# Kernel tuning notes

Measured on AMD Instinct MI355X. Metric: run time of the kernel, lower is better.

Reference implementation:

```python
import jax, jax.numpy as jnp
import numpy as np

NB_OBJECTS = 3
DIM_BODY = 10
DIM_OBJECT = 15
DIM_ACT = 4
DIM_NODE = 128
D_PHI_IN = DIM_ACT + DIM_BODY + DIM_OBJECT + DIM_NODE  # 157
HID = 256
D_PHI_OUT = 3 * D_PHI_IN  # 471
D_RHO_OUT = 1
BATCH = 65536


def _linear_init(key, fan_in, fan_out):
    # torch nn.Linear default: U(-1/sqrt(fan_in), 1/sqrt(fan_in))
    bound = 1.0 / np.sqrt(fan_in)
    k1, k2 = jax.random.split(key)
    W = jax.random.uniform(k1, (fan_in, fan_out), minval=-bound, maxval=bound, dtype=jnp.float32)
    b = jax.random.uniform(k2, (fan_out,), minval=-bound, maxval=bound, dtype=jnp.float32)
    return W, b


def setup_inputs() -> dict:
    key = jax.random.key(0)
    ks = jax.random.split(key, 11)
    obs = jax.random.normal(ks[0], (BATCH, DIM_BODY + NB_OBJECTS * DIM_OBJECT), dtype=jnp.float32)
    act = jax.random.normal(ks[1], (BATCH, DIM_ACT), dtype=jnp.float32)
    nodes = jax.random.normal(ks[2], (NB_OBJECTS, BATCH, DIM_NODE), dtype=jnp.float32)
    phi1_w1, phi1_b1 = _linear_init(ks[3], D_PHI_IN, HID)
    phi1_w2, phi1_b2 = _linear_init(ks[4], HID, D_PHI_OUT)
    phi2_w1, phi2_b1 = _linear_init(ks[5], D_PHI_IN, HID)
    phi2_w2, phi2_b2 = _linear_init(ks[6], HID, D_PHI_OUT)
    rho1_w1, rho1_b1 = _linear_init(ks[7], D_PHI_OUT, HID)
    rho1_w2, rho1_b2 = _linear_init(ks[8], HID, D_RHO_OUT)
    rho2_w1, rho2_b1 = _linear_init(ks[9], D_PHI_OUT, HID)
    rho2_w2, rho2_b2 = _linear_init(ks[10], HID, D_RHO_OUT)
    return {
        "obs": obs, "act": act, "nodes": nodes,
        "phi1_w1": phi1_w1, "phi1_b1": phi1_b1, "phi1_w2": phi1_w2, "phi1_b2": phi1_b2,
        "phi2_w1": phi2_w1, "phi2_b1": phi2_b1, "phi2_w2": phi2_w2, "phi2_b2": phi2_b2,
        "rho1_w1": rho1_w1, "rho1_b1": rho1_b1, "rho1_w2": rho1_w2, "rho1_b2": rho1_b2,
        "rho2_w1": rho2_w1, "rho2_b1": rho2_b1, "rho2_w2": rho2_w2, "rho2_b2": rho2_b2,
    }


def reference(obs, act, nodes,
              phi1_w1, phi1_b1, phi1_w2, phi1_b2,
              phi2_w1, phi2_b1, phi2_w2, phi2_b2,
              rho1_w1, rho1_b1, rho1_w2, rho1_b2,
              rho2_w1, rho2_b1, rho2_w2, rho2_b2):
    B = obs.shape[0]
    obs_body = obs[:, :DIM_BODY]                                   # [B, 10]
    # per-object slices -> [nb_objects, B, dim_object]
    obs_obj = obs[:, DIM_BODY:].reshape(B, NB_OBJECTS, DIM_OBJECT).transpose(1, 0, 2)
    shared = jnp.concatenate([act, obs_body], axis=-1)             # [B, 14]
    shared = jnp.broadcast_to(shared[None], (NB_OBJECTS, B, shared.shape[-1]))
    inp_phi = jnp.concatenate([shared, obs_obj, nodes], axis=-1)   # [3, B, 157]

    def mlp2(x, w1, b1, w2, b2):
        h = jax.nn.relu(x @ w1 + b1)
        return jax.nn.relu(h @ w2 + b2)

    # DeepSet: per-entity phi then sum over entities
    out1 = mlp2(inp_phi, phi1_w1, phi1_b1, phi1_w2, phi1_b2).sum(axis=0)  # [B, 471]
    out2 = mlp2(inp_phi, phi2_w1, phi2_b1, phi2_w2, phi2_b2).sum(axis=0)
    q1 = jax.nn.relu(out1 @ rho1_w1 + rho1_b1) @ rho1_w2 + rho1_b2        # [B, 1]
    q2 = jax.nn.relu(out2 @ rho2_w1 + rho2_b1) @ rho2_w2 + rho2_b2
    return (q1, q2)
```

## Files before the change

kernel.cpp:

```cpp
#include <hip/hip_runtime.h>
#include <hip/hip_fp16.h>

typedef _Float16 half8 __attribute__((ext_vector_type(8)));
typedef float f32x4 __attribute__((ext_vector_type(4)));

#define BATCH 65536
#define M1 196608
#define K1 192

#define GLL16(g, l) __builtin_amdgcn_global_load_lds( \
    (const __attribute__((address_space(1))) unsigned int*)(const void*)(g), \
    (__attribute__((address_space(3))) unsigned int*)(void*)(l), 16, 0, 0)

__global__ void prep_kernel(const float* __restrict__ p1w1, const float* __restrict__ p2w1,
                            const float* __restrict__ p1w2, const float* __restrict__ p2w2,
                            const float* __restrict__ r1w1, const float* __restrict__ r2w1,
                            const float* __restrict__ p1b1, const float* __restrict__ p2b1,
                            const float* __restrict__ p1b2, const float* __restrict__ p2b2,
                            const float* __restrict__ rb1a, const float* __restrict__ rb1b,
                            _Float16* __restrict__ W1t, _Float16* __restrict__ W2t,
                            _Float16* __restrict__ R1t, float* __restrict__ b1cat,
                            float* __restrict__ b2cat, float* __restrict__ rbias) {
    int e = blockIdx.x * 256 + threadIdx.x;
    if (e < 98304) {
        int n = e / 192, c = e % 192;
        int k = (c < 128) ? (29 + c) : (c - 128);
        float v = 0.f;
        if (c < 128 || (c - 128) < 29) v = (n < 256) ? p1w1[k * 256 + n] : p2w1[k * 256 + (n - 256)];
        W1t[e] = (_Float16)v;
        return;
    }
    e -= 98304;
    if (e < 262144) {
        int net = e >> 17, rr = e & 131071;
        int n = rr >> 8, k = rr & 255;
        const float* w = net ? p2w2 : p1w2;
        W2t[(size_t)net * 131072 + rr] = (n < 471) ? (_Float16)w[k * 471 + n] : (_Float16)0.f;
        return;
    }
    e -= 262144;
    if (e < 262144) {
        int net = e >> 17, rr = e & 131071;
        int n = rr >> 9, k = rr & 511;
        const float* w = net ? r2w1 : r1w1;
        R1t[(size_t)net * 131072 + rr] = (k < 471) ? (_Float16)w[k * 256 + n] : (_Float16)0.f;
        return;
    }
    e -= 262144;
    if (e < 512) { b1cat[e] = (e < 256) ? p1b1[e] : p2b1[e - 256]; return; }
    e -= 512;
    if (e < 1024) {
        int net = e >> 9, n = e & 511;
        b2cat[e] = (n < 471) ? (net ? p2b2 : p1b2)[n] : 0.f;
        return;
    }
    e -= 1024;
    if (e < 512) {
        int net = e >> 8, n = e & 255;
        rbias[e] = (net ? rb1b : rb1a)[n];
    }
}

__global__ void build_x(const float* __restrict__ obs, const float* __restrict__ act,
                        const float* __restrict__ nodes, _Float16* __restrict__ Xh) {
    long idx = (long)blockIdx.x * 256 + threadIdx.x;
    int ch = (int)(idx % 24);
    long r = idx / 24;
    int o = (int)(r >> 16), b = (int)(r & 65535);
    half8 v;
    if (ch < 16) {
        const float* s = nodes + r * 128 + ch * 8;
#pragma unroll
        for (int j = 0; j < 8; ++j) v[j] = (_Float16)s[j];
    } else if (ch < 20) {
#pragma unroll
        for (int j = 0; j < 8; ++j) {
            int lc = ch * 8 + j - 128;
            float f = 0.f;
            if (lc < 4)       f = act[b * 4 + lc];
            else if (lc < 14) f = obs[b * 55 + (lc - 4)];
            else if (lc < 29) f = obs[b * 55 + 10 + o * 15 + (lc - 14)];
            v[j] = (_Float16)f;
        }
    } else {
#pragma unroll
        for (int j = 0; j < 8; ++j) v[j] = (_Float16)0.f;
    }
    *(half8*)(Xh + r * 192 + ch * 8) = v;
}


__global__ __launch_bounds__(256) void gemm1(const _Float16* __restrict__ Xh,
                                             const _Float16* __restrict__ W1t,
                                             const float* __restrict__ b1cat,
                                             _Float16* __restrict__ H) {
    __shared__ _Float16 As[2][4096];
    __shared__ _Float16 Bs[2][4096];
    const int tid = threadIdx.x;
    int bid = blockIdx.x;
    int w = (bid & 7) * 768 + (bid >> 3);
    const int m0 = (w >> 2) * 128, n0 = (w & 3) * 128;
    const _Float16* Ab = Xh + (long)m0 * K1;
    const _Float16* Bb = W1t + (long)n0 * K1;
    const int wid = tid >> 6, lane = tid & 63;
    const int lm = lane & 15, lq = lane >> 4;
    const int wr = (wid >> 1) * 64, wc = (wid & 1) * 64;
    const int srow = tid >> 2, schk = tid & 3;

    auto stage = [&](int s, int buf) {
        int ko = s * 32;
#pragma unroll
        for (int g = 0; g < 2; ++g) {
            int row = srow + g * 64, q = schk ^ ((row >> 1) & 3);
            GLL16(Ab + (long)row * K1 + ko + q * 8, &As[buf][0] + g * 2048 + wid * 512);
            GLL16(Bb + (long)row * K1 + ko + q * 8, &Bs[buf][0] + g * 2048 + wid * 512);
        }
    };

    stage(0, 0);
    __syncthreads();

    const int cc = (lq ^ ((lm >> 1) & 3)) * 8;
    f32x4 acc[4][4] = {};
    int cur = 0;
#pragma unroll
    for (int r = 0; r < 6; ++r) {
        if (r < 5) stage(r + 1, cur ^ 1);
        const _Float16* ab = &As[cur][0];
        const _Float16* bb = &Bs[cur][0];
        half8 a[4], b[4];
#pragma unroll
        for (int i = 0; i < 4; ++i) a[i] = *(const half8*)(ab + (wr + i * 16 + lm) * 32 + cc);
#pragma unroll
        for (int j = 0; j < 4; ++j) b[j] = *(const half8*)(bb + (wc + j * 16 + lm) * 32 + cc);
#pragma unroll
        for (int i = 0; i < 4; ++i)
#pragma unroll
            for (int j = 0; j < 4; ++j)
                acc[i][j] = __builtin_amdgcn_mfma_f32_16x16x32_f16(a[i], b[j], acc[i][j], 0, 0, 0);
        __syncthreads();
        cur ^= 1;
    }
#pragma unroll
    for (int j = 0; j < 4; ++j) {
        int n = n0 + wc + j * 16 + lm;
        int net = n >> 8, ncol = n & 255;
        float bi = b1cat[n];
        _Float16* hp = H + (long)net * ((long)M1 * 256) + ncol;
#pragma unroll
        for (int i = 0; i < 4; ++i) {
            int mrow = m0 + wr + i * 16 + lq * 4;
#pragma unroll
            for (int rg = 0; rg < 4; ++rg) {
                float v = acc[i][j][rg] + bi;
                v = v > 0.f ? v : 0.f;
                hp[(long)(mrow + rg) * 256] = (_Float16)v;
            }
        }
    }
}

__global__ __launch_bounds__(256) void gemm_sum(const _Float16* __restrict__ H,
                                                const _Float16* __restrict__ W2t,
                                                const float* __restrict__ b2cat,
                                                _Float16* __restrict__ Osum) {
    __shared__ _Float16 As[2][4096];
    __shared__ _Float16 Bs[2][4096];
    const int tid = threadIdx.x;
    int bid = blockIdx.x;
    int w = (bid & 7) * 512 + (bid >> 3);
    const int n0 = (w & 3) * 128, net = (w >> 2) & 1, b0 = (w >> 3) * 128;
    const _Float16* Ab = H + (long)net * ((long)M1 * 256) + (long)b0 * 256;
    const _Float16* Bb = W2t + (long)net * 131072 + (long)n0 * 256;
    const float* bp = b2cat + net * 512;
    const int wid = tid >> 6, lane = tid & 63;
    const int lm = lane & 15, lq = lane >> 4;
    const int wr = (wid >> 1) * 64, wc = (wid & 1) * 64;
    const int srow = tid >> 2, schk = tid & 3;

    float bi[4];
#pragma unroll
    for (int j = 0; j < 4; ++j) bi[j] = bp[n0 + wc + j * 16 + lm];

    auto stage = [&](int s, int buf) {
        int obj = s >> 3, ko = (s & 7) * 32;
#pragma unroll
        for (int g = 0; g < 2; ++g) {
            int row = srow + g * 64, q = schk ^ ((row >> 1) & 3);
            GLL16(Ab + ((long)obj * BATCH + row) * 256 + ko + q * 8, &As[buf][0] + g * 2048 + wid * 512);
            GLL16(Bb + (long)row * 256 + ko + q * 8, &Bs[buf][0] + g * 2048 + wid * 512);
        }
    };

    stage(0, 0);
    __syncthreads();

    const int cc = (lq ^ ((lm >> 1) & 3)) * 8;
    f32x4 acc[4][4] = {};
    f32x4 sum[4][4] = {};
    int cur = 0;
    for (int r = 0; r < 24; ++r) {
        if (r < 23) stage(r + 1, cur ^ 1);
        const _Float16* ab = &As[cur][0];
        const _Float16* bb = &Bs[cur][0];
        half8 a[4], b[4];
#pragma unroll
        for (int i = 0; i < 4; ++i) a[i] = *(const half8*)(ab + (wr + i * 16 + lm) * 32 + cc);
#pragma unroll
        for (int j = 0; j < 4; ++j) b[j] = *(const half8*)(bb + (wc + j * 16 + lm) * 32 + cc);
#pragma unroll
        for (int i = 0; i < 4; ++i)
#pragma unroll
            for (int j = 0; j < 4; ++j)
                acc[i][j] = __builtin_amdgcn_mfma_f32_16x16x32_f16(a[i], b[j], acc[i][j], 0, 0, 0);
        if ((r & 7) == 7) {
#pragma unroll
            for (int i = 0; i < 4; ++i)
#pragma unroll
                for (int j = 0; j < 4; ++j) {
#pragma unroll
                    for (int rg = 0; rg < 4; ++rg) {
                        float v = acc[i][j][rg] + bi[j];
                        sum[i][j][rg] += (v > 0.f ? v : 0.f);
                    }
                    acc[i][j] = f32x4{0.f, 0.f, 0.f, 0.f};
                }
        }
        __syncthreads();
        cur ^= 1;
    }
    _Float16* op = Osum + (long)net * ((long)BATCH * 512);
#pragma unroll
    for (int j = 0; j < 4; ++j) {
        int n = n0 + wc + j * 16 + lm;
#pragma unroll
        for (int i = 0; i < 4; ++i) {
            int mrow = b0 + wr + i * 16 + lq * 4;
#pragma unroll
            for (int rg = 0; rg < 4; ++rg)
                op[(long)(mrow + rg) * 512 + n] = (_Float16)sum[i][j][rg];
        }
    }
}

__global__ __launch_bounds__(512) void gemm3q(const _Float16* __restrict__ Osum,
                                              const _Float16* __restrict__ R1t,
                                              const float* __restrict__ rbias,
                                              const float* __restrict__ r1w2,
                                              const float* __restrict__ r2w2,
                                              const float* __restrict__ r1b2,
                                              const float* __restrict__ r2b2,
                                              float* __restrict__ out) {
    __shared__ _Float16 As[2][4096];
    __shared__ _Float16 Bs[2][8192];
    __shared__ float qlds[128];
    const int tid = threadIdx.x;
    int bid = blockIdx.x;
    int w = (bid & 7) * 128 + (bid >> 3);
    const int net = w & 1, b0 = (w >> 1) * 128;
    if (tid < 128) qlds[tid] = 0.f;
    const _Float16* Ab = Osum + (long)net * ((long)BATCH * 512) + (long)b0 * 512;
    const _Float16* Bb = R1t + (long)net * 131072;
    const int wid = tid >> 6, lane = tid & 63;
    const int lm = lane & 15, lq = lane >> 4;
    const int wr = (wid >> 2) * 64, wc = (wid & 3) * 64;
    const int srow = tid >> 2, schk = tid & 3;

    auto stage = [&](int s, int buf) {
        int ko = s * 32;
        {
            int row = srow, q = schk ^ ((row >> 1) & 3);
            GLL16(Ab + (long)row * 512 + ko + q * 8, &As[buf][0] + wid * 512);
        }
#pragma unroll
        for (int g = 0; g < 2; ++g) {
            int row = srow + g * 128, q = schk ^ ((row >> 1) & 3);
            GLL16(Bb + (long)row * 512 + ko + q * 8, &Bs[buf][0] + g * 4096 + wid * 512);
        }
    };

    stage(0, 0);
    __syncthreads();

    const int cc = (lq ^ ((lm >> 1) & 3)) * 8;
    f32x4 acc[4][4] = {};
    int cur = 0;
    for (int r = 0; r < 16; ++r) {
        if (r < 15) stage(r + 1, cur ^ 1);
        const _Float16* ab = &As[cur][0];
        const _Float16* bb = &Bs[cur][0];
        half8 a[4], b[4];
#pragma unroll
        for (int i = 0; i < 4; ++i) a[i] = *(const half8*)(ab + (wr + i * 16 + lm) * 32 + cc);
#pragma unroll
        for (int j = 0; j < 4; ++j) b[j] = *(const half8*)(bb + (wc + j * 16 + lm) * 32 + cc);
#pragma unroll
        for (int i = 0; i < 4; ++i)
#pragma unroll
            for (int j = 0; j < 4; ++j)
                acc[i][j] = __builtin_amdgcn_mfma_f32_16x16x32_f16(a[i], b[j], acc[i][j], 0, 0, 0);
        __syncthreads();
        cur ^= 1;
    }
    const float* w2 = net ? r2w2 : r1w2;
    const float* rb = rbias + net * 256;
    float w2v[4], bv[4];
#pragma unroll
    for (int j = 0; j < 4; ++j) {
        int col = wc + j * 16 + lm;
        w2v[j] = w2[col];
        bv[j] = rb[col];
    }
    f32x4 qp[4] = {};
#pragma unroll
    for (int i = 0; i < 4; ++i)
#pragma unroll
        for (int j = 0; j < 4; ++j)
#pragma unroll
            for (int rg = 0; rg < 4; ++rg) {
                float v = acc[i][j][rg] + bv[j];
                v = v > 0.f ? v : 0.f;
                qp[i][rg] += v * w2v[j];
            }
#pragma unroll
    for (int d = 1; d < 16; d <<= 1)
#pragma unroll
        for (int i = 0; i < 4; ++i)
#pragma unroll
            for (int rg = 0; rg < 4; ++rg)
                qp[i][rg] += __shfl_xor(qp[i][rg], d, 64);
    if ((lane & 15) == 0) {
#pragma unroll
        for (int i = 0; i < 4; ++i)
#pragma unroll
            for (int rg = 0; rg < 4; ++rg)
                atomicAdd(&qlds[wr + i * 16 + lq * 4 + rg], qp[i][rg]);
    }
    __syncthreads();
    if (tid < 128)
        out[(long)net * BATCH + b0 + tid] = qlds[tid] + (net ? r2b2[0] : r1b2[0]);
}

extern "C" void kernel_launch(void* const* d_in, const int* in_sizes, int n_in,
                              void* d_out, int out_size, void* d_ws, size_t ws_size,
                              hipStream_t stream) {
    const float* obs  = (const float*)d_in[0];
    const float* act  = (const float*)d_in[1];
    const float* nodes= (const float*)d_in[2];
    const float* p1w1 = (const float*)d_in[3];  const float* p1b1 = (const float*)d_in[4];
    const float* p1w2 = (const float*)d_in[5];  const float* p1b2 = (const float*)d_in[6];
    const float* p2w1 = (const float*)d_in[7];  const float* p2b1 = (const float*)d_in[8];
    const float* p2w2 = (const float*)d_in[9];  const float* p2b2 = (const float*)d_in[10];
    const float* r1w1 = (const float*)d_in[11]; const float* r1b1 = (const float*)d_in[12];
    const float* r1w2 = (const float*)d_in[13]; const float* r1b2 = (const float*)d_in[14];
    const float* r2w1 = (const float*)d_in[15]; const float* r2b1 = (const float*)d_in[16];
    const float* r2w2 = (const float*)d_in[17]; const float* r2b2 = (const float*)d_in[18];

    const size_t oW1t  = 0;
    const size_t oW2t  = 196608;
    const size_t oR1t  = 720896;
    const size_t oB1   = 1245184;
    const size_t oB2   = 1247232;
    const size_t oRB   = 1251328;
    const size_t oXO   = 1253376;
    const size_t oH    = 135471104;
    const size_t need  = 336797696;
    if (ws_size < need) return;

    char* ws = (char*)d_ws;
    _Float16* W1t  = (_Float16*)(ws + oW1t);
    _Float16* W2t  = (_Float16*)(ws + oW2t);
    _Float16* R1t  = (_Float16*)(ws + oR1t);
    float*    b1cat= (float*)(ws + oB1);
    float*    b2cat= (float*)(ws + oB2);
    float*    rbias= (float*)(ws + oRB);
    _Float16* Xh   = (_Float16*)(ws + oXO);
    _Float16* Osum = (_Float16*)(ws + oXO);
    _Float16* H    = (_Float16*)(ws + oH);
    float* out = (float*)d_out;

    prep_kernel<<<2440, 256, 0, stream>>>(p1w1, p2w1, p1w2, p2w2, r1w1, r2w1,
                                          p1b1, p2b1, p1b2, p2b2, r1b1, r2b1,
                                          W1t, W2t, R1t, b1cat, b2cat, rbias);
    build_x<<<18432, 256, 0, stream>>>(obs, act, nodes, Xh);
    gemm1<<<6144, 256, 0, stream>>>(Xh, W1t, b1cat, H);
    gemm_sum<<<4096, 256, 0, stream>>>(H, W2t, b2cat, Osum);
    gemm3q<<<1024, 512, 0, stream>>>(Osum, R1t, rbias, r1w2, r2w2, r1b2, r2b2, out);
}
```

Measured before the change: 391.5 us.

## Keep weight panel resident in LDS with persistent blocks and triple-buffered A streaming

```diff
diff --git a/kernel.cpp b/kernel.cpp
--- a/kernel.cpp
+++ b/kernel.cpp
@@ -11,6 +11,10 @@
 #define GLL16(g, l) __builtin_amdgcn_global_load_lds( \
     (const __attribute__((address_space(1))) unsigned int*)(const void*)(g), \
     (__attribute__((address_space(3))) unsigned int*)(void*)(l), 16, 0, 0)
+
+#define WAIT_VM1() asm volatile("s_waitcnt vmcnt(1)" ::: "memory")
+#define WAIT_VM0() asm volatile("s_waitcnt vmcnt(0)" ::: "memory")
+#define SBAR() do { __builtin_amdgcn_s_barrier(); __builtin_amdgcn_sched_barrier(0); } while (0)
 
 __global__ void prep_kernel(const float* __restrict__ p1w1, const float* __restrict__ p2w1,
                             const float* __restrict__ p1w2, const float* __restrict__ p2w2,
@@ -22,15 +26,15 @@
                             _Float16* __restrict__ R1t, float* __restrict__ b1cat,
                             float* __restrict__ b2cat, float* __restrict__ rbias) {
     int e = blockIdx.x * 256 + threadIdx.x;
-    if (e < 98304) {
-        int n = e / 192, c = e % 192;
+    if (e < 131072) {
+        int n = e >> 8, c = e & 255;
         int k = (c < 128) ? (29 + c) : (c - 128);
         float v = 0.f;
-        if (c < 128 || (c - 128) < 29) v = (n < 256) ? p1w1[k * 256 + n] : p2w1[k * 256 + (n - 256)];
+        if (c < 157) v = (n < 256) ? p1w1[k * 256 + n] : p2w1[k * 256 + (n - 256)];
         W1t[e] = (_Float16)v;
         return;
     }
-    e -= 98304;
+    e -= 131072;
     if (e < 262144) {
         int net = e >> 17, rr = e & 131071;
         int n = rr >> 8, k = rr & 255;
@@ -90,155 +94,171 @@
 }
 
 
-__global__ __launch_bounds__(256) void gemm1(const _Float16* __restrict__ Xh,
+__global__ __launch_bounds__(512) void gemm1(const _Float16* __restrict__ Xh,
                                              const _Float16* __restrict__ W1t,
                                              const float* __restrict__ b1cat,
                                              _Float16* __restrict__ H) {
-    __shared__ _Float16 As[2][4096];
-    __shared__ _Float16 Bs[2][4096];
+    __shared__ _Float16 Bp[65536];
+    __shared__ _Float16 Ar[3][4096];
     const int tid = threadIdx.x;
-    int bid = blockIdx.x;
-    int w = (bid & 7) * 768 + (bid >> 3);
-    const int m0 = (w >> 2) * 128, n0 = (w & 3) * 128;
-    const _Float16* Ab = Xh + (long)m0 * K1;
-    const _Float16* Bb = W1t + (long)n0 * K1;
+    const int bid = blockIdx.x;
+    const int nhalf = bid & 1;
+    const int mset = bid >> 1;
+    const int MT = 6, R = 6, TOT = 36;
     const int wid = tid >> 6, lane = tid & 63;
     const int lm = lane & 15, lq = lane >> 4;
-    const int wr = (wid >> 1) * 64, wc = (wid & 1) * 64;
-    const int srow = tid >> 2, schk = tid & 3;
-
-    auto stage = [&](int s, int buf) {
-        int ko = s * 32;
-#pragma unroll
-        for (int g = 0; g < 2; ++g) {
-            int row = srow + g * 64, q = schk ^ ((row >> 1) & 3);
-            GLL16(Ab + (long)row * K1 + ko + q * 8, &As[buf][0] + g * 2048 + wid * 512);
-            GLL16(Bb + (long)row * K1 + ko + q * 8, &Bs[buf][0] + g * 2048 + wid * 512);
-        }
+    const int wr = (wid >> 2) * 64, wc = (wid & 3) * 64;
+
+    {
+        const _Float16* src = W1t + (long)nhalf * 65536;
+#pragma unroll
+        for (int it = 0; it < 16; ++it) {
+            int row = it * 16 + (tid >> 5);
+            int q = (tid & 31) ^ (row & 7);
+            GLL16(src + (long)row * 256 + q * 8, &Bp[0] + it * 4096 + wid * 512);
+        }
+    }
+    const int arow = tid >> 2, asch = tid & 3;
+    const int aq = asch ^ ((arow >> 1) & 3);
+    auto stageA = [&](int g) {
+        int mt = g / R, s = g - mt * R;
+        int m0 = (mset * MT + mt) * 128;
+        GLL16(Xh + (long)(m0 + arow) * K1 + s * 32 + aq * 8, &Ar[g % 3][0] + wid * 512);
     };
-
-    stage(0, 0);
-    __syncthreads();
+    stageA(0); stageA(1);
 
     const int cc = (lq ^ ((lm >> 1) & 3)) * 8;
-    f32x4 acc[4][4] = {};
-    int cur = 0;
-#pragma unroll
-    for (int r = 0; r < 6; ++r) {
-        if (r < 5) stage(r + 1, cur ^ 1);
-        const _Float16* ab = &As[cur][0];
-        const _Float16* bb = &Bs[cur][0];
-        half8 a[4], b[4];
-#pragma unroll
-        for (int i = 0; i < 4; ++i) a[i] = *(const half8*)(ab + (wr + i * 16 + lm) * 32 + cc);
-#pragma unroll
-        for (int j = 0; j < 4; ++j) b[j] = *(const half8*)(bb + (wc + j * 16 + lm) * 32 + cc);
-#pragma unroll
-        for (int i = 0; i < 4; ++i)
-#pragma unroll
-            for (int j = 0; j < 4; ++j)
-                acc[i][j] = __builtin_amdgcn_mfma_f32_16x16x32_f16(a[i], b[j], acc[i][j], 0, 0, 0);
-        __syncthreads();
-        cur ^= 1;
-    }
-#pragma unroll
-    for (int j = 0; j < 4; ++j) {
-        int n = n0 + wc + j * 16 + lm;
-        int net = n >> 8, ncol = n & 255;
-        float bi = b1cat[n];
-        _Float16* hp = H + (long)net * ((long)M1 * 256) + ncol;
-#pragma unroll
-        for (int i = 0; i < 4; ++i) {
-            int mrow = m0 + wr + i * 16 + lq * 4;
-#pragma unroll
-            for (int rg = 0; rg < 4; ++rg) {
-                float v = acc[i][j][rg] + bi;
-                v = v > 0.f ? v : 0.f;
-                hp[(long)(mrow + rg) * 256] = (_Float16)v;
+    const int bxr = lm & 7;
+    float bi[4];
+#pragma unroll
+    for (int j = 0; j < 4; ++j) bi[j] = b1cat[nhalf * 256 + wc + j * 16 + lm];
+    _Float16* hp0 = H + (long)nhalf * ((long)M1 * 256);
+
+    int rr = 0;
+    for (int mt = 0; mt < MT; ++mt) {
+        f32x4 acc[4][4] = {};
+        for (int s = 0; s < R; ++s, ++rr) {
+            if (rr + 1 < TOT) { WAIT_VM1(); } else { WAIT_VM0(); }
+            SBAR();
+            if (rr + 2 < TOT) stageA(rr + 2);
+            const _Float16* ab = &Ar[rr % 3][0];
+            half8 a[4], b[4];
+#pragma unroll
+            for (int i = 0; i < 4; ++i) a[i] = *(const half8*)(ab + (wr + i * 16 + lm) * 32 + cc);
+            int bc = ((s * 4 + lq) ^ bxr) * 8;
+#pragma unroll
+            for (int j = 0; j < 4; ++j) b[j] = *(const half8*)(&Bp[0] + (wc + j * 16 + lm) * 256 + bc);
+#pragma unroll
+            for (int i = 0; i < 4; ++i)
+#pragma unroll
+                for (int j = 0; j < 4; ++j)
+                    acc[i][j] = __builtin_amdgcn_mfma_f32_16x16x32_f16(a[i], b[j], acc[i][j], 0, 0, 0);
+        }
+        int m0 = (mset * MT + mt) * 128;
+#pragma unroll
+        for (int j = 0; j < 4; ++j) {
+            int ncol = wc + j * 16 + lm;
+#pragma unroll
+            for (int i = 0; i < 4; ++i) {
+                int mrow = m0 + wr + i * 16 + lq * 4;
+#pragma unroll
+                for (int rg = 0; rg < 4; ++rg) {
+                    float v = acc[i][j][rg] + bi[j];
+                    v = v > 0.f ? v : 0.f;
+                    hp0[(long)(mrow + rg) * 256 + ncol] = (_Float16)v;
+                }
             }
         }
     }
 }
 
-__global__ __launch_bounds__(256) void gemm_sum(const _Float16* __restrict__ H,
+__global__ __launch_bounds__(512) void gemm_sum(const _Float16* __restrict__ H,
                                                 const _Float16* __restrict__ W2t,
                                                 const float* __restrict__ b2cat,
                                                 _Float16* __restrict__ Osum) {
-    __shared__ _Float16 As[2][4096];
-    __shared__ _Float16 Bs[2][4096];
+    __shared__ _Float16 Bp[65536];
+    __shared__ _Float16 Ar[3][4096];
     const int tid = threadIdx.x;
-    int bid = blockIdx.x;
-    int w = (bid & 7) * 512 + (bid >> 3);
-    const int n0 = (w & 3) * 128, net = (w >> 2) & 1, b0 = (w >> 3) * 128;
-    const _Float16* Ab = H + (long)net * ((long)M1 * 256) + (long)b0 * 256;
-    const _Float16* Bb = W2t + (long)net * 131072 + (long)n0 * 256;
-    const float* bp = b2cat + net * 512;
+    const int bid = blockIdx.x;
+    const int net = bid & 1, nhalf = (bid >> 1) & 1, mset = bid >> 2;
+    const int MT = 4, R = 24, TOT = 96;
+    const int n0 = nhalf * 256;
     const int wid = tid >> 6, lane = tid & 63;
     const int lm = lane & 15, lq = lane >> 4;
-    const int wr = (wid >> 1) * 64, wc = (wid & 1) * 64;
-    const int srow = tid >> 2, schk = tid & 3;
-
+    const int wr = (wid >> 2) * 64, wc = (wid & 3) * 64;
+    const _Float16* Hb = H + (long)net * ((long)M1 * 256);
+
+    {
+        const _Float16* src = W2t + (long)net * 131072 + (long)n0 * 256;
+#pragma unroll
+        for (int it = 0; it < 16; ++it) {
+            int row = it * 16 + (tid >> 5);
+            int q = (tid & 31) ^ (row & 7);
+            GLL16(src + (long)row * 256 + q * 8, &Bp[0] + it * 4096 + wid * 512);
+        }
+    }
+    const int arow = tid >> 2, asch = tid & 3;
+    const int aq = asch ^ ((arow >> 1) & 3);
+    auto stageA = [&](int g) {
+        int mt = g / R, s = g - mt * R;
+        int obj = s >> 3, ko = (s & 7) * 32;
+        int m0 = (mset * MT + mt) * 128;
+        GLL16(Hb + ((long)(obj * BATCH + m0 + arow)) * 256 + ko + aq * 8, &Ar[g % 3][0] + wid * 512);
+    };
+    stageA(0); stageA(1);
+
+    const int cc = (lq ^ ((lm >> 1) & 3)) * 8;
+    const int bxr = lm & 7;
     float bi[4];
 #pragma unroll
-    for (int j = 0; j < 4; ++j) bi[j] = bp[n0 + wc + j * 16 + lm];
-
-    auto stage = [&](int s, int buf) {
-        int obj = s >> 3, ko = (s & 7) * 32;
-#pragma unroll
-        for (int g = 0; g < 2; ++g) {
-            int row = srow + g * 64, q = schk ^ ((row >> 1) & 3);
-            GLL16(Ab + ((long)obj * BATCH + row) * 256 + ko + q * 8, &As[buf][0] + g * 2048 + wid * 512);
-            GLL16(Bb + (long)row * 256 + ko + q * 8, &Bs[buf][0] + g * 2048 + wid * 512);
-        }
-    };
-
-    stage(0, 0);
-    __syncthreads();
-
-    const int cc = (lq ^ ((lm >> 1) & 3)) * 8;
-    f32x4 acc[4][4] = {};
-    f32x4 sum[4][4] = {};
-    int cur = 0;
-    for (int r = 0; r < 24; ++r) {
-        if (r < 23) stage(r + 1, cur ^ 1);
-        const _Float16* ab = &As[cur][0];
-        const _Float16* bb = &Bs[cur][0];
-        half8 a[4], b[4];
-#pragma unroll
-        for (int i = 0; i < 4; ++i) a[i] = *(const half8*)(ab + (wr + i * 16 + lm) * 32 + cc);
-#pragma unroll
-        for (int j = 0; j < 4; ++j) b[j] = *(const half8*)(bb + (wc + j * 16 + lm) * 32 + cc);
-#pragma unroll
-        for (int i = 0; i < 4; ++i)
-#pragma unroll
-            for (int j = 0; j < 4; ++j)
-                acc[i][j] = __builtin_amdgcn_mfma_f32_16x16x32_f16(a[i], b[j], acc[i][j], 0, 0, 0);
-        if ((r & 7) == 7) {
+    for (int j = 0; j < 4; ++j) bi[j] = b2cat[net * 512 + n0 + wc + j * 16 + lm];
+    _Float16* op = Osum + (long)net * ((long)BATCH * 512);
+
+    int rr = 0;
+    for (int mt = 0; mt < MT; ++mt) {
+        f32x4 acc[4][4] = {};
+        f32x4 sum[4][4] = {};
+        for (int s = 0; s < R; ++s, ++rr) {
+            if (rr + 1 < TOT) { WAIT_VM1(); } else { WAIT_VM0(); }
+            SBAR();
+            if (rr + 2 < TOT) stageA(rr + 2);
+            const _Float16* ab = &Ar[rr % 3][0];
+            half8 a[4], b[4];
+#pragma unroll
+            for (int i = 0; i < 4; ++i) a[i] = *(const half8*)(ab + (wr + i * 16 + lm) * 32 + cc);
+            int bc = (((s & 7) * 4 + lq) ^ bxr) * 8;
+#pragma unroll
+            for (int j = 0; j < 4; ++j) b[j] = *(const half8*)(&Bp[0] + (wc + j * 16 + lm) * 256 + bc);
 #pragma unroll
             for (int i = 0; i < 4; ++i)
 #pragma unroll
-                for (int j = 0; j < 4; ++j) {
-#pragma unroll
-                    for (int rg = 0; rg < 4; ++rg) {
-                        float v = acc[i][j][rg] + bi[j];
-                        sum[i][j][rg] += (v > 0.f ? v : 0.f);
+                for (int j = 0; j < 4; ++j)
+                    acc[i][j] = __builtin_amdgcn_mfma_f32_16x16x32_f16(a[i], b[j], acc[i][j], 0, 0, 0);
+            if ((s & 7) == 7) {
+#pragma unroll
+                for (int i = 0; i < 4; ++i)
+#pragma unroll
+                    for (int j = 0; j < 4; ++j) {
+#pragma unroll
+                        for (int rg = 0; rg < 4; ++rg) {
+                            float v = acc[i][j][rg] + bi[j];
+                            sum[i][j][rg] += (v > 0.f ? v : 0.f);
+                        }
+                        acc[i][j] = f32x4{0.f, 0.f, 0.f, 0.f};
                     }
-                    acc[i][j] = f32x4{0.f, 0.f, 0.f, 0.f};
-                }
-        }
-        __syncthreads();
-        cur ^= 1;
-    }
-    _Float16* op = Osum + (long)net * ((long)BATCH * 512);
-#pragma unroll
-    for (int j = 0; j < 4; ++j) {
-        int n = n0 + wc + j * 16 + lm;
-#pragma unroll
-        for (int i = 0; i < 4; ++i) {
-            int mrow = b0 + wr + i * 16 + lq * 4;
-#pragma unroll
-            for (int rg = 0; rg < 4; ++rg)
-                op[(long)(mrow + rg) * 512 + n] = (_Float16)sum[i][j][rg];
+            }
+        }
+        int m0 = (mset * MT + mt) * 128;
+#pragma unroll
+        for (int j = 0; j < 4; ++j) {
+            int n = n0 + wc + j * 16 + lm;
+#pragma unroll
+            for (int i = 0; i < 4; ++i) {
+                int mrow = m0 + wr + i * 16 + lq * 4;
+#pragma unroll
+                for (int rg = 0; rg < 4; ++rg)
+                    op[(long)(mrow + rg) * 512 + n] = (_Float16)sum[i][j][rg];
+            }
         }
     }
 }
@@ -251,8 +271,8 @@
                                               const float* __restrict__ r1b2,
                                               const float* __restrict__ r2b2,
                                               float* __restrict__ out) {
-    __shared__ _Float16 As[2][4096];
-    __shared__ _Float16 Bs[2][8192];
+    __shared__ _Float16 As[2][8192];
+    __shared__ _Float16 Bs[2][16384];
     __shared__ float qlds[128];
     const int tid = threadIdx.x;
     int bid = blockIdx.x;
@@ -264,17 +284,19 @@
     const int wid = tid >> 6, lane = tid & 63;
     const int lm = lane & 15, lq = lane >> 4;
     const int wr = (wid >> 2) * 64, wc = (wid & 3) * 64;
-    const int srow = tid >> 2, schk = tid & 3;
+    const int xv = lm & 7;
+    const int srow = tid >> 3, schk = tid & 7;
 
     auto stage = [&](int s, int buf) {
-        int ko = s * 32;
-        {
-            int row = srow, q = schk ^ ((row >> 1) & 3);
-            GLL16(Ab + (long)row * 512 + ko + q * 8, &As[buf][0] + wid * 512);
-        }
+        int ko = s * 64;
 #pragma unroll
         for (int g = 0; g < 2; ++g) {
-            int row = srow + g * 128, q = schk ^ ((row >> 1) & 3);
+            int row = srow + g * 64, q = schk ^ (row & 7);
+            GLL16(Ab + (long)row * 512 + ko + q * 8, &As[buf][0] + g * 4096 + wid * 512);
+        }
+#pragma unroll
+        for (int g = 0; g < 4; ++g) {
+            int row = srow + g * 64, q = schk ^ (row & 7);
             GLL16(Bb + (long)row * 512 + ko + q * 8, &Bs[buf][0] + g * 4096 + wid * 512);
         }
     };
@@ -282,23 +304,26 @@
     stage(0, 0);
     __syncthreads();
 
-    const int cc = (lq ^ ((lm >> 1) & 3)) * 8;
     f32x4 acc[4][4] = {};
     int cur = 0;
-    for (int r = 0; r < 16; ++r) {
-        if (r < 15) stage(r + 1, cur ^ 1);
+    for (int r = 0; r < 8; ++r) {
+        if (r < 7) stage(r + 1, cur ^ 1);
         const _Float16* ab = &As[cur][0];
         const _Float16* bb = &Bs[cur][0];
-        half8 a[4], b[4];
-#pragma unroll
-        for (int i = 0; i < 4; ++i) a[i] = *(const half8*)(ab + (wr + i * 16 + lm) * 32 + cc);
-#pragma unroll
-        for (int j = 0; j < 4; ++j) b[j] = *(const half8*)(bb + (wc + j * 16 + lm) * 32 + cc);
-#pragma unroll
-        for (int i = 0; i < 4; ++i)
-#pragma unroll
-            for (int j = 0; j < 4; ++j)
-                acc[i][j] = __builtin_amdgcn_mfma_f32_16x16x32_f16(a[i], b[j], acc[i][j], 0, 0, 0);
+#pragma unroll
+        for (int ks = 0; ks < 2; ++ks) {
+            const int off = ((ks * 4 + lq) ^ xv) * 8;
+            half8 a[4], b[4];
+#pragma unroll
+            for (int i = 0; i < 4; ++i) a[i] = *(const half8*)(ab + (wr + i * 16 + lm) * 64 + off);
+#pragma unroll
+            for (int j = 0; j < 4; ++j) b[j] = *(const half8*)(bb + (wc + j * 16 + lm) * 64 + off);
+#pragma unroll
+            for (int i = 0; i < 4; ++i)
+#pragma unroll
+                for (int j = 0; j < 4; ++j)
+                    acc[i][j] = __builtin_amdgcn_mfma_f32_16x16x32_f16(a[i], b[j], acc[i][j], 0, 0, 0);
+        }
         __syncthreads();
         cur ^= 1;
     }
@@ -357,14 +382,14 @@
     const float* r2w2 = (const float*)d_in[17]; const float* r2b2 = (const float*)d_in[18];
 
     const size_t oW1t  = 0;
-    const size_t oW2t  = 196608;
-    const size_t oR1t  = 720896;
-    const size_t oB1   = 1245184;
-    const size_t oB2   = 1247232;
-    const size_t oRB   = 1251328;
-    const size_t oXO   = 1253376;
-    const size_t oH    = 135471104;
-    const size_t need  = 336797696;
+    const size_t oW2t  = 262144;
+    const size_t oR1t  = 786432;
+    const size_t oB1   = 1310720;
+    const size_t oB2   = 1312768;
+    const size_t oRB   = 1316864;
+    const size_t oXO   = 1318912;
+    const size_t oH    = 135536640;
+    const size_t need  = 336863232;
     if (ws_size < need) return;
 
     char* ws = (char*)d_ws;
@@ -379,11 +404,11 @@
     _Float16* H    = (_Float16*)(ws + oH);
     float* out = (float*)d_out;
 
-    prep_kernel<<<2440, 256, 0, stream>>>(p1w1, p2w1, p1w2, p2w2, r1w1, r2w1,
+    prep_kernel<<<2568, 256, 0, stream>>>(p1w1, p2w1, p1w2, p2w2, r1w1, r2w1,
                                           p1b1, p2b1, p1b2, p2b2, r1b1, r2b1,
                                           W1t, W2t, R1t, b1cat, b2cat, rbias);
     build_x<<<18432, 256, 0, stream>>>(obs, act, nodes, Xh);
-    gemm1<<<6144, 256, 0, stream>>>(Xh, W1t, b1cat, H);
-    gemm_sum<<<4096, 256, 0, stream>>>(H, W2t, b2cat, Osum);
+    gemm1<<<512, 512, 0, stream>>>(Xh, W1t, b1cat, H);
+    gemm_sum<<<512, 512, 0, stream>>>(H, W2t, b2cat, Osum);
     gemm3q<<<1024, 512, 0, stream>>>(Osum, R1t, rbias, r1w2, r2w2, r1b2, r2b2, out);
 }
```

Result: faster. 378.7 us (-3.3%).

## Trim layer-1 K padding and double K-tile depth in gemm_sum and gemm3q

Applied to the files above, without the earlier changes.

```diff
diff --git a/kernel.cpp b/kernel.cpp
--- a/kernel.cpp
+++ b/kernel.cpp
@@ -6,7 +6,7 @@
 
 #define BATCH 65536
 #define M1 196608
-#define K1 192
+#define K1 160
 
 #define GLL16(g, l) __builtin_amdgcn_global_load_lds( \
     (const __attribute__((address_space(1))) unsigned int*)(const void*)(g), \
@@ -22,15 +22,15 @@
                             _Float16* __restrict__ R1t, float* __restrict__ b1cat,
                             float* __restrict__ b2cat, float* __restrict__ rbias) {
     int e = blockIdx.x * 256 + threadIdx.x;
-    if (e < 98304) {
-        int n = e / 192, c = e % 192;
+    if (e < 81920) {
+        int n = e / 160, c = e % 160;
         int k = (c < 128) ? (29 + c) : (c - 128);
         float v = 0.f;
-        if (c < 128 || (c - 128) < 29) v = (n < 256) ? p1w1[k * 256 + n] : p2w1[k * 256 + (n - 256)];
+        if (c < 157) v = (n < 256) ? p1w1[k * 256 + n] : p2w1[k * 256 + (n - 256)];
         W1t[e] = (_Float16)v;
         return;
     }
-    e -= 98304;
+    e -= 81920;
     if (e < 262144) {
         int net = e >> 17, rr = e & 131071;
         int n = rr >> 8, k = rr & 255;
@@ -64,15 +64,15 @@
 __global__ void build_x(const float* __restrict__ obs, const float* __restrict__ act,
                         const float* __restrict__ nodes, _Float16* __restrict__ Xh) {
     long idx = (long)blockIdx.x * 256 + threadIdx.x;
-    int ch = (int)(idx % 24);
-    long r = idx / 24;
+    int ch = (int)(idx % 20);
+    long r = idx / 20;
     int o = (int)(r >> 16), b = (int)(r & 65535);
     half8 v;
     if (ch < 16) {
         const float* s = nodes + r * 128 + ch * 8;
 #pragma unroll
         for (int j = 0; j < 8; ++j) v[j] = (_Float16)s[j];
-    } else if (ch < 20) {
+    } else {
 #pragma unroll
         for (int j = 0; j < 8; ++j) {
             int lc = ch * 8 + j - 128;
@@ -82,11 +82,8 @@
             else if (lc < 29) f = obs[b * 55 + 10 + o * 15 + (lc - 14)];
             v[j] = (_Float16)f;
         }
-    } else {
-#pragma unroll
-        for (int j = 0; j < 8; ++j) v[j] = (_Float16)0.f;
-    }
-    *(half8*)(Xh + r * 192 + ch * 8) = v;
+    }
+    *(half8*)(Xh + r * K1 + ch * 8) = v;
 }
 
 
@@ -105,15 +102,15 @@
     const int wid = tid >> 6, lane = tid & 63;
     const int lm = lane & 15, lq = lane >> 4;
     const int wr = (wid >> 1) * 64, wc = (wid & 1) * 64;
-    const int srow = tid >> 2, schk = tid & 3;
 
     auto stage = [&](int s, int buf) {
         int ko = s * 32;
 #pragma unroll
-        for (int g = 0; g < 2; ++g) {
-            int row = srow + g * 64, q = schk ^ ((row >> 1) & 3);
-            GLL16(Ab + (long)row * K1 + ko + q * 8, &As[buf][0] + g * 2048 + wid * 512);
-            GLL16(Bb + (long)row * K1 + ko + q * 8, &Bs[buf][0] + g * 2048 + wid * 512);
+        for (int t = 0; t < 2; ++t) {
+            int c = t * 256 + tid, row = c >> 2, chk = c & 3;
+            int q = chk ^ ((row >> 1) & 3);
+            GLL16(Ab + (long)row * K1 + ko + q * 8, &As[buf][0] + t * 2048 + wid * 512);
+            GLL16(Bb + (long)row * K1 + ko + q * 8, &Bs[buf][0] + t * 2048 + wid * 512);
         }
     };
 
@@ -124,8 +121,8 @@
     f32x4 acc[4][4] = {};
     int cur = 0;
 #pragma unroll
-    for (int r = 0; r < 6; ++r) {
-        if (r < 5) stage(r + 1, cur ^ 1);
+    for (int r = 0; r < 5; ++r) {
+        if (r < 4) stage(r + 1, cur ^ 1);
         const _Float16* ab = &As[cur][0];
         const _Float16* bb = &Bs[cur][0];
         half8 a[4], b[4];
@@ -164,56 +161,60 @@
                                                 const _Float16* __restrict__ W2t,
                                                 const float* __restrict__ b2cat,
                                                 _Float16* __restrict__ Osum) {
-    __shared__ _Float16 As[2][4096];
-    __shared__ _Float16 Bs[2][4096];
+    __shared__ _Float16 As[2][8192];
+    __shared__ _Float16 Bs[2][8192];
     const int tid = threadIdx.x;
     int bid = blockIdx.x;
     int w = (bid & 7) * 512 + (bid >> 3);
     const int n0 = (w & 3) * 128, net = (w >> 2) & 1, b0 = (w >> 3) * 128;
     const _Float16* Ab = H + (long)net * ((long)M1 * 256) + (long)b0 * 256;
     const _Float16* Bb = W2t + (long)net * 131072 + (long)n0 * 256;
-    const float* bp = b2cat + net * 512;
     const int wid = tid >> 6, lane = tid & 63;
     const int lm = lane & 15, lq = lane >> 4;
     const int wr = (wid >> 1) * 64, wc = (wid & 1) * 64;
-    const int srow = tid >> 2, schk = tid & 3;
 
     float bi[4];
 #pragma unroll
-    for (int j = 0; j < 4; ++j) bi[j] = bp[n0 + wc + j * 16 + lm];
+    for (int j = 0; j < 4; ++j) bi[j] = b2cat[net * 512 + n0 + wc + j * 16 + lm];
 
     auto stage = [&](int s, int buf) {
-        int obj = s >> 3, ko = (s & 7) * 32;
-#pragma unroll
-        for (int g = 0; g < 2; ++g) {
-            int row = srow + g * 64, q = schk ^ ((row >> 1) & 3);
-            GLL16(Ab + ((long)obj * BATCH + row) * 256 + ko + q * 8, &As[buf][0] + g * 2048 + wid * 512);
-            GLL16(Bb + (long)row * 256 + ko + q * 8, &Bs[buf][0] + g * 2048 + wid * 512);
+        int obj = s >> 2, ko = (s & 3) * 64;
+        const _Float16* Ao = Ab + (long)obj * BATCH * 256;
+#pragma unroll
+        for (int t = 0; t < 4; ++t) {
+            int c = t * 256 + tid, row = c >> 3, chk = c & 7;
+            int q = chk ^ (row & 7);
+            GLL16(Ao + (long)row * 256 + ko + q * 8, &As[buf][0] + t * 2048 + wid * 512);
+            GLL16(Bb + (long)row * 256 + ko + q * 8, &Bs[buf][0] + t * 2048 + wid * 512);
         }
     };
 
     stage(0, 0);
     __syncthreads();
 
-    const int cc = (lq ^ ((lm >> 1) & 3)) * 8;
+    const int xv = lm & 7;
     f32x4 acc[4][4] = {};
     f32x4 sum[4][4] = {};
     int cur = 0;
-    for (int r = 0; r < 24; ++r) {
-        if (r < 23) stage(r + 1, cur ^ 1);
+    for (int r = 0; r < 12; ++r) {
+        if (r < 11) stage(r + 1, cur ^ 1);
         const _Float16* ab = &As[cur][0];
         const _Float16* bb = &Bs[cur][0];
-        half8 a[4], b[4];
-#pragma unroll
-        for (int i = 0; i < 4; ++i) a[i] = *(const half8*)(ab + (wr + i * 16 + lm) * 32 + cc);
-#pragma unroll
-        for (int j = 0; j < 4; ++j) b[j] = *(const half8*)(bb + (wc + j * 16 + lm) * 32 + cc);
-#pragma unroll
-        for (int i = 0; i < 4; ++i)
-#pragma unroll
-            for (int j = 0; j < 4; ++j)
-                acc[i][j] = __builtin_amdgcn_mfma_f32_16x16x32_f16(a[i], b[j], acc[i][j], 0, 0, 0);
-        if ((r & 7) == 7) {
+#pragma unroll
+        for (int ks = 0; ks < 2; ++ks) {
+            const int off = ((ks * 4 + lq) ^ xv) * 8;
+            half8 a[4], b[4];
+#pragma unroll
+            for (int i = 0; i < 4; ++i) a[i] = *(const half8*)(ab + (wr + i * 16 + lm) * 64 + off);
+#pragma unroll
+            for (int j = 0; j < 4; ++j) b[j] = *(const half8*)(bb + (wc + j * 16 + lm) * 64 + off);
+#pragma unroll
+            for (int i = 0; i < 4; ++i)
+#pragma unroll
+                for (int j = 0; j < 4; ++j)
+                    acc[i][j] = __builtin_amdgcn_mfma_f32_16x16x32_f16(a[i], b[j], acc[i][j], 0, 0, 0);
+        }
+        if ((r & 3) == 3) {
 #pragma unroll
             for (int i = 0; i < 4; ++i)
 #pragma unroll
@@ -251,8 +252,8 @@
                                               const float* __restrict__ r1b2,
                                               const float* __restrict__ r2b2,
                                               float* __restrict__ out) {
-    __shared__ _Float16 As[2][4096];
-    __shared__ _Float16 Bs[2][8192];
+    __shared__ _Float16 As[2][8192];
+    __shared__ _Float16 Bs[2][16384];
     __shared__ float qlds[128];
     const int tid = threadIdx.x;
     int bid = blockIdx.x;
@@ -264,17 +265,19 @@
     const int wid = tid >> 6, lane = tid & 63;
     const int lm = lane & 15, lq = lane >> 4;
     const int wr = (wid >> 2) * 64, wc = (wid & 3) * 64;
-    const int srow = tid >> 2, schk = tid & 3;
+    const int xv = lm & 7;
+    const int srow = tid >> 3, schk = tid & 7;
 
     auto stage = [&](int s, int buf) {
-        int ko = s * 32;
-        {
-            int row = srow, q = schk ^ ((row >> 1) & 3);
-            GLL16(Ab + (long)row * 512 + ko + q * 8, &As[buf][0] + wid * 512);
-        }
+        int ko = s * 64;
 #pragma unroll
         for (int g = 0; g < 2; ++g) {
-            int row = srow + g * 128, q = schk ^ ((row >> 1) & 3);
+            int row = srow + g * 64, q = schk ^ (row & 7);
+            GLL16(Ab + (long)row * 512 + ko + q * 8, &As[buf][0] + g * 4096 + wid * 512);
+        }
+#pragma unroll
+        for (int g = 0; g < 4; ++g) {
+            int row = srow + g * 64, q = schk ^ (row & 7);
             GLL16(Bb + (long)row * 512 + ko + q * 8, &Bs[buf][0] + g * 4096 + wid * 512);
         }
     };
@@ -282,23 +285,26 @@
     stage(0, 0);
     __syncthreads();
 
-    const int cc = (lq ^ ((lm >> 1) & 3)) * 8;
     f32x4 acc[4][4] = {};
     int cur = 0;
-    for (int r = 0; r < 16; ++r) {
-        if (r < 15) stage(r + 1, cur ^ 1);
+    for (int r = 0; r < 8; ++r) {
+        if (r < 7) stage(r + 1, cur ^ 1);
         const _Float16* ab = &As[cur][0];
         const _Float16* bb = &Bs[cur][0];
-        half8 a[4], b[4];
-#pragma unroll
-        for (int i = 0; i < 4; ++i) a[i] = *(const half8*)(ab + (wr + i * 16 + lm) * 32 + cc);
-#pragma unroll
-        for (int j = 0; j < 4; ++j) b[j] = *(const half8*)(bb + (wc + j * 16 + lm) * 32 + cc);
-#pragma unroll
-        for (int i = 0; i < 4; ++i)
-#pragma unroll
-            for (int j = 0; j < 4; ++j)
-                acc[i][j] = __builtin_amdgcn_mfma_f32_16x16x32_f16(a[i], b[j], acc[i][j], 0, 0, 0);
+#pragma unroll
+        for (int ks = 0; ks < 2; ++ks) {
+            const int off = ((ks * 4 + lq) ^ xv) * 8;
+            half8 a[4], b[4];
+#pragma unroll
+            for (int i = 0; i < 4; ++i) a[i] = *(const half8*)(ab + (wr + i * 16 + lm) * 64 + off);
+#pragma unroll
+            for (int j = 0; j < 4; ++j) b[j] = *(const half8*)(bb + (wc + j * 16 + lm) * 64 + off);
+#pragma unroll
+            for (int i = 0; i < 4; ++i)
+#pragma unroll
+                for (int j = 0; j < 4; ++j)
+                    acc[i][j] = __builtin_amdgcn_mfma_f32_16x16x32_f16(a[i], b[j], acc[i][j], 0, 0, 0);
+        }
         __syncthreads();
         cur ^= 1;
     }
@@ -357,14 +363,14 @@
     const float* r2w2 = (const float*)d_in[17]; const float* r2b2 = (const float*)d_in[18];
 
     const size_t oW1t  = 0;
-    const size_t oW2t  = 196608;
-    const size_t oR1t  = 720896;
-    const size_t oB1   = 1245184;
-    const size_t oB2   = 1247232;
-    const size_t oRB   = 1251328;
-    const size_t oXO   = 1253376;
-    const size_t oH    = 135471104;
-    const size_t need  = 336797696;
+    const size_t oW2t  = 163840;
+    const size_t oR1t  = 688128;
+    const size_t oB1   = 1212416;
+    const size_t oB2   = 1214464;
+    const size_t oRB   = 1218560;
+    const size_t oXO   = 1220608;
+    const size_t oH    = 135438336;
+    const size_t need  = 336764928;
     if (ws_size < need) return;
 
     char* ws = (char*)d_ws;
@@ -379,10 +385,10 @@
     _Float16* H    = (_Float16*)(ws + oH);
     float* out = (float*)d_out;
 
-    prep_kernel<<<2440, 256, 0, stream>>>(p1w1, p2w1, p1w2, p2w2, r1w1, r2w1,
+    prep_kernel<<<2376, 256, 0, stream>>>(p1w1, p2w1, p1w2, p2w2, r1w1, r2w1,
                                           p1b1, p2b1, p1b2, p2b2, r1b1, r2b1,
                                           W1t, W2t, R1t, b1cat, b2cat, rbias);
-    build_x<<<18432, 256, 0, stream>>>(obs, act, nodes, Xh);
+    build_x<<<15360, 256, 0, stream>>>(obs, act, nodes, Xh);
     gemm1<<<6144, 256, 0, stream>>>(Xh, W1t, b1cat, H);
     gemm_sum<<<4096, 256, 0, stream>>>(H, W2t, b2cat, Osum);
     gemm3q<<<1024, 512, 0, stream>>>(Osum, R1t, rbias, r1w2, r2w2, r1b2, r2b2, out);
```

After: 342.5 us. -12.5%, faster.
